# Performance work log

Measured on AMD Instinct MI355X. Metric: run time of the kernel, lower is better.

Reference implementation:

```python
import jax, jax.numpy as jnp
import numpy as np

TINY = 1e-6

def _norm(x):
    return x / (jnp.linalg.norm(x, axis=-1, keepdims=True) + TINY)

def setup_inputs() -> dict:
    key = jax.random.key(0)
    ks = jax.random.split(key, 8)
    N, L, S, H = 8192, 128, 8, 16
    points = jax.random.normal(ks[0], (N, 3), dtype=jnp.float32)
    normals = _norm(jax.random.normal(ks[1], (N, 3), dtype=jnp.float32))
    # orthonormal root rotation (world -> canonical)
    root_rot, _ = jnp.linalg.qr(jax.random.normal(ks[2], (3, 3), dtype=jnp.float32))
    lgtSGLobes = jax.random.normal(ks[3], (L, 3), dtype=jnp.float32)
    # SG sharpness must be > 1 so arccos(1 - 1/lambda) is well defined
    lgtSGLambdas = jax.random.uniform(ks[4], (L, 1), dtype=jnp.float32) * 30.0 + 5.0
    r_theta_random = jax.random.uniform(ks[5], (N, L, S), dtype=jnp.float32)
    W1 = jax.random.normal(ks[6], (6, H), dtype=jnp.float32) * 0.5
    b1 = jnp.zeros((H,), dtype=jnp.float32)
    W2 = jax.random.normal(ks[7], (H, 1), dtype=jnp.float32) * 0.5
    b2 = jnp.zeros((1,), dtype=jnp.float32)
    return {"points": points, "normals": normals, "root_rot": root_rot,
            "lgtSGLobes": lgtSGLobes, "lgtSGLambdas": lgtSGLambdas,
            "r_theta_random": r_theta_random, "W1": W1, "b1": b1, "W2": W2, "b2": b2}

def reference(points, normals, root_rot, lgtSGLobes, lgtSGLambdas,
              r_theta_random, W1, b1, W2, b2):
    # points/normals: [N,3]; lgtSGLobes: [L,3]; r_theta_random: [N,L,S]
    N = points.shape[0]
    L, S = r_theta_random.shape[1], r_theta_random.shape[2]
    l = _norm(lgtSGLobes)                                  # [L,3] SG lobe axes
    z = jnp.zeros_like(l).at[:, 2].set(1.0)
    U = _norm(jnp.cross(z, l))                             # local frame around lobe
    V = _norm(jnp.cross(l, U))
    sharp = lgtSGLambdas[:, 0]                             # [L]
    r_phi = jnp.clip(jnp.arccos(1.0 - 1.0 / sharp), None, np.pi / 3.0)  # [L]
    lin = (jnp.arange(S, dtype=points.dtype) / S)          # stratified offsets
    r_theta = (r_theta_random / S + lin) * (2.0 * np.pi)   # [N,L,S]
    st, ct = jnp.sin(r_theta), jnp.cos(r_theta)            # [N,L,S]
    sp, cp = jnp.sin(r_phi), jnp.cos(r_phi)                # [L]
    # importance-sampled directions around each lobe: [N,L,S,3]
    sample_dir = (U[None, :, None, :] * (ct * sp[None, :, None])[..., None]
                  + V[None, :, None, :] * (st * sp[None, :, None])[..., None]
                  + l[None, :, None, :] * cp[None, :, None, None])
    # hemisphere mask (normals . sample_dir > eps)
    cos_term = jnp.einsum('nd,nlsd->nls', normals, sample_dir) > TINY
    # rotate query dirs to canonical frame: (-dir) @ root_rot
    input_dir = jnp.einsum('nlsd,de->nlse', -sample_dir, root_rot)
    # visibility MLP on (point, dir); concat avoided by splitting W1
    h = jax.nn.relu(jnp.einsum('nlsd,dh->nlsh', input_dir, W1[3:])
                    + (points @ W1[:3])[:, None, None, :] + b1)   # [N,L,S,H]
    pred_vis = jax.nn.sigmoid(jnp.einsum('nlsh,ho->nlso', h, W2)[..., 0] + b2[0])
    vis = jnp.where(cos_term, pred_vis, 0.0)               # masked scatter-back
    # SG weights exp(lambda*(dir.lobe - 1)); weighted reduction over samples
    w = jnp.exp(sharp[None, :, None] * (jnp.einsum('nlsd,ld->nls', sample_dir, l) - 1.0))
    return jnp.sum(vis * w, axis=-1) / (jnp.sum(w, axis=-1) + TINY)  # [N,L]
```

## Files before the change

kernel.cpp:

```cpp
#include <hip/hip_runtime.h>
#include <math.h>

typedef _Float16 h2 __attribute__((ext_vector_type(2)));
typedef __fp16  hh2 __attribute__((ext_vector_type(2)));

constexpr int Lc = 128;
constexpr int Sc = 8;
constexpr int F0_OFF = 3072;
constexpr int F1_OFF = 3584;
constexpr int WQ_OFF = 4096;
constexpr int W2_OFF = 4224;
constexpr int B2_OFF = 4232;
constexpr int PB_OFF = 4352;

static __device__ __forceinline__ h2 pk(float a, float b) {
    return __builtin_bit_cast(h2, __builtin_amdgcn_cvt_pkrtz(a, b));
}
static __device__ __forceinline__ h2 u2h(unsigned u) {
    return __builtin_bit_cast(h2, u);
}
static __device__ __forceinline__ unsigned h2u(h2 v) {
    return __builtin_bit_cast(unsigned, v);
}
static __device__ __forceinline__ float fdot2f(h2 a, h2 b, float c) {
#if __has_builtin(__builtin_amdgcn_fdot2)
    return __builtin_amdgcn_fdot2(__builtin_bit_cast(hh2, a),
                                  __builtin_bit_cast(hh2, b), c, false);
#else
    return c + (float)a.x * (float)b.x + (float)a.y * (float)b.y;
#endif
}
static __device__ __forceinline__ float fast_exp2(float x) {
#if __has_builtin(__builtin_amdgcn_exp2f)
    return __builtin_amdgcn_exp2f(x);
#else
    return exp2f(x);
#endif
}

__global__ __launch_bounds__(256) void precompute(
    const float* __restrict__ points,
    const float* __restrict__ root_rot,
    const float* __restrict__ lobes,
    const float* __restrict__ lambdas,
    const float* __restrict__ W1,
    const float* __restrict__ b1,
    const float* __restrict__ W2,
    const float* __restrict__ b2,
    unsigned* __restrict__ ws, int N)
{
    int g = blockIdx.x * 256 + threadIdx.x;

    if (g < N) {
        float px = points[3*g], py = points[3*g+1], pz = points[3*g+2];
        unsigned* dst = ws + PB_OFF + 8*(size_t)g;
        #pragma unroll
        for (int k = 0; k < 8; ++k) {
            int h0 = 2*k, h1 = 2*k+1;
            float v0 = b1[h0] + px*W1[h0] + py*W1[16+h0] + pz*W1[32+h0];
            float v1 = b1[h1] + px*W1[h1] + py*W1[16+h1] + pz*W1[32+h1];
            dst[k] = h2u(pk(v0, v1));
        }
    }

    if (g < Lc) {
        int li = g;
        float lx = lobes[li*3+0], ly = lobes[li*3+1], lz = lobes[li*3+2];
        float inv = 1.0f / (sqrtf(lx*lx + ly*ly + lz*lz) + 1e-6f);
        lx *= inv; ly *= inv; lz *= inv;

        float ux = -ly, uy = lx;
        inv = 1.0f / (sqrtf(ux*ux + uy*uy) + 1e-6f);
        ux *= inv; uy *= inv;

        float vx = -lz*uy, vy = lz*ux, vz = lx*uy - ly*ux;
        inv = 1.0f / (sqrtf(vx*vx + vy*vy + vz*vz) + 1e-6f);
        vx *= inv; vy *= inv; vz *= inv;

        float sharp = lambdas[li];
        float cp = fmaxf(1.0f - 1.0f/sharp, 0.5f);
        float sp = sqrtf(fmaxf(1.0f - cp*cp, 0.0f));

        float uxs = ux*sp, uys = uy*sp;
        float vxs = vx*sp, vys = vy*sp, vzs = vz*sp;
        float lxc = lx*cp, lyc = ly*cp, lzc = lz*cp;

        const float r0 = root_rot[0], r1 = root_rot[1], r2 = root_rot[2];
        const float r3 = root_rot[3], r4 = root_rot[4], r5 = root_rot[5];
        const float r6 = root_rot[6], r7 = root_rot[7], r8 = root_rot[8];

        float Ur0 = -(uxs*r0 + uys*r3);
        float Ur1 = -(uxs*r1 + uys*r4);
        float Ur2 = -(uxs*r2 + uys*r5);
        float Vr0 = -(vxs*r0 + vys*r3 + vzs*r6);
        float Vr1 = -(vxs*r1 + vys*r4 + vzs*r7);
        float Vr2 = -(vxs*r2 + vys*r5 + vzs*r8);
        float Lr0 = -(lxc*r0 + lyc*r3 + lzc*r6);
        float Lr1 = -(lxc*r1 + lyc*r4 + lzc*r7);
        float Lr2 = -(lxc*r2 + lyc*r5 + lzc*r8);

        unsigned abd[24];
        #pragma unroll
        for (int k = 0; k < 8; ++k) {
            int h0 = 2*k, h1 = 2*k + 1;
            float a0 = Ur0*W1[48+h0] + Ur1*W1[64+h0] + Ur2*W1[80+h0];
            float a1 = Ur0*W1[48+h1] + Ur1*W1[64+h1] + Ur2*W1[80+h1];
            float bb0 = Vr0*W1[48+h0] + Vr1*W1[64+h0] + Vr2*W1[80+h0];
            float bb1 = Vr0*W1[48+h1] + Vr1*W1[64+h1] + Vr2*W1[80+h1];
            float d0 = Lr0*W1[48+h0] + Lr1*W1[64+h0] + Lr2*W1[80+h0];
            float d1 = Lr0*W1[48+h1] + Lr1*W1[64+h1] + Lr2*W1[80+h1];
            abd[k]      = h2u(pk(a0, a1));
            abd[8 + k]  = h2u(pk(bb0, bb1));
            abd[16 + k] = h2u(pk(d0, d1));
        }
        uint4* tv = (uint4*)ws;
        #pragma unroll
        for (int c = 0; c < 6; ++c)
            tv[c*128 + li] = *(const uint4*)(abd + 4*c);

        float* wf = (float*)ws;
        *(float4*)(wf + F0_OFF + 4*li) = (float4){uxs, uys, vxs, vys};
        *(float4*)(wf + F1_OFF + 4*li) = (float4){vzs, lxc, lyc, lzc};
        float wq = __expf(sharp * (cp - 1.0f));
        wf[WQ_OFF + li] = wq / (8.0f * wq + 1e-6f);

        if (li == 0) {
            #pragma unroll
            for (int k = 0; k < 8; ++k)
                ws[W2_OFF + k] = h2u(pk(W2[2*k], W2[2*k+1]));
            wf[B2_OFF] = -b2[0] * 1.44269504f;
        }
    }
}

__global__ __launch_bounds__(256, 4) void vis_main(
    const float* __restrict__ normals,
    const float* __restrict__ rtheta,
    const unsigned* __restrict__ ws,
    float* __restrict__ out, int N)
{
    int idx = blockIdx.x * 256 + threadIdx.x;
    if (idx >= N * Lc) return;
    int n  = idx >> 7;
    int li = idx & (Lc - 1);

    const uint4* tv = (const uint4*)ws;
    uint4 a01 = tv[0*128 + li];
    uint4 a23 = tv[1*128 + li];
    uint4 bb01 = tv[2*128 + li];
    uint4 bb23 = tv[3*128 + li];
    uint4 d01 = tv[4*128 + li];
    uint4 d23 = tv[5*128 + li];
    const float* wf = (const float*)ws;
    float4 f0 = *(const float4*)(wf + F0_OFF + 4*li);
    float4 f1 = *(const float4*)(wf + F1_OFF + 4*li);
    float wqp = wf[WQ_OFF + li];

    const float4 q0 = *reinterpret_cast<const float4*>(rtheta + (size_t)idx * Sc);
    const float4 q1 = *reinterpret_cast<const float4*>(rtheta + (size_t)idx * Sc + 4);
    float rs[Sc] = {q0.x, q0.y, q0.z, q0.w, q1.x, q1.y, q1.z, q1.w};

    int nu = __builtin_amdgcn_readfirstlane(n);
    const float* nn = normals + 3*(size_t)nu;
    float nx = nn[0], ny = nn[1], nz = nn[2];
    const unsigned* pbp = ws + PB_OFF + 8*(size_t)nu;
    unsigned pb[8] = {pbp[0], pbp[1], pbp[2], pbp[3],
                      pbp[4], pbp[5], pbp[6], pbp[7]};

    h2 A[8] = {u2h(a01.x), u2h(a01.y), u2h(a01.z), u2h(a01.w),
               u2h(a23.x), u2h(a23.y), u2h(a23.z), u2h(a23.w)};
    h2 B[8] = {u2h(bb01.x), u2h(bb01.y), u2h(bb01.z), u2h(bb01.w),
               u2h(bb23.x), u2h(bb23.y), u2h(bb23.z), u2h(bb23.w)};
    h2 G[8] = {u2h(pb[0]) + u2h(d01.x), u2h(pb[1]) + u2h(d01.y),
               u2h(pb[2]) + u2h(d01.z), u2h(pb[3]) + u2h(d01.w),
               u2h(pb[4]) + u2h(d23.x), u2h(pb[5]) + u2h(d23.y),
               u2h(pb[6]) + u2h(d23.z), u2h(pb[7]) + u2h(d23.w)};
    h2 W2h[8] = {u2h(ws[W2_OFF+0]), u2h(ws[W2_OFF+1]),
                 u2h(ws[W2_OFF+2]), u2h(ws[W2_OFF+3]),
                 u2h(ws[W2_OFF+4]), u2h(ws[W2_OFF+5]),
                 u2h(ws[W2_OFF+6]), u2h(ws[W2_OFF+7])};
    float b2c = wf[B2_OFF];

    float nU = nx*f0.x + ny*f0.y;
    float nV = nx*f0.z + ny*f0.w + nz*f1.x;
    float nL = nx*f1.y + ny*f1.z + nz*f1.w;

    const h2 zero = {(_Float16)0.0f, (_Float16)0.0f};
    float svis = 0.0f;
    #pragma unroll
    for (int s = 0; s < Sc; ++s) {
        float f  = fmaf(rs[s], 0.125f, (float)s * 0.125f);
        float st = __builtin_amdgcn_sinf(f);
        float ct = __builtin_amdgcn_cosf(f);
        float ndot = fmaf(ct, nU, fmaf(st, nV, nL));

        h2 ct2 = pk(ct, ct);
        h2 st2 = pk(st, st);

        float acc = 0.0f;
        #pragma unroll
        for (int k = 0; k < 8; ++k) {
            h2 hv = __builtin_elementwise_fma(ct2, A[k],
                     __builtin_elementwise_fma(st2, B[k], G[k]));
            hv = __builtin_elementwise_max(hv, zero);
            acc = fdot2f(hv, W2h[k], acc);
        }
        float e = fast_exp2(fmaf(acc, -1.44269504f, b2c));
        float pred = __builtin_amdgcn_rcpf(1.0f + e);
        svis += (ndot > 1e-6f) ? pred : 0.0f;
    }

    out[idx] = svis * wqp;
}

extern "C" void kernel_launch(void* const* d_in, const int* in_sizes, int n_in,
                              void* d_out, int out_size, void* d_ws, size_t ws_size,
                              hipStream_t stream) {
    const float* points  = (const float*)d_in[0];
    const float* normals = (const float*)d_in[1];
    const float* root_rot= (const float*)d_in[2];
    const float* lobes   = (const float*)d_in[3];
    const float* lambdas = (const float*)d_in[4];
    const float* rtheta  = (const float*)d_in[5];
    const float* W1      = (const float*)d_in[6];
    const float* b1      = (const float*)d_in[7];
    const float* W2      = (const float*)d_in[8];
    const float* b2      = (const float*)d_in[9];
    float* out = (float*)d_out;
    unsigned* ws = (unsigned*)d_ws;

    int N = in_sizes[0] / 3;
    int total = N * Lc;

    int pre_blocks = (N + 255) / 256;
    precompute<<<pre_blocks, 256, 0, stream>>>(points, root_rot, lobes, lambdas,
                                               W1, b1, W2, b2, ws, N);
    vis_main<<<(total + 255) / 256, 256, 0, stream>>>(normals, rtheta, ws, out, N);
}
```

Before: 24.88 us.

## Fuse precompute into main kernel with per-block LDS tables

Removes the separate precompute launch. Each block now recomputes the per-lobe frame and MLP projection tables into shared memory, splitting the hidden units across its two halves, plus the point bias for its two points. The main computation then reads these tables from LDS instead of a global workspace. This drops one kernel launch and the global round trip, at the cost of redundant per-block setup work (lobe normalization and W1 projections in every block) and a __syncthreads barrier.

```diff
diff --git a/kernel.cpp b/kernel.cpp
--- a/kernel.cpp
+++ b/kernel.cpp
@@ -6,12 +6,11 @@
 
 constexpr int Lc = 128;
 constexpr int Sc = 8;
-constexpr int F0_OFF = 3072;
-constexpr int F1_OFF = 3584;
+
+constexpr int F_OFF  = 3072;
 constexpr int WQ_OFF = 4096;
-constexpr int W2_OFF = 4224;
-constexpr int B2_OFF = 4232;
-constexpr int PB_OFF = 4352;
+constexpr int PB_OFF = 4224;
+constexpr int LDS_DW = 4240;
 
 static __device__ __forceinline__ h2 pk(float a, float b) {
     return __builtin_bit_cast(h2, __builtin_amdgcn_cvt_pkrtz(a, b));
@@ -38,33 +37,24 @@
 #endif
 }
 
-__global__ __launch_bounds__(256) void precompute(
+__global__ __launch_bounds__(256, 4) void vis_fused(
     const float* __restrict__ points,
+    const float* __restrict__ normals,
     const float* __restrict__ root_rot,
     const float* __restrict__ lobes,
     const float* __restrict__ lambdas,
+    const float* __restrict__ rtheta,
     const float* __restrict__ W1,
     const float* __restrict__ b1,
     const float* __restrict__ W2,
     const float* __restrict__ b2,
-    unsigned* __restrict__ ws, int N)
+    float* __restrict__ out, int N)
 {
-    int g = blockIdx.x * 256 + threadIdx.x;
-
-    if (g < N) {
-        float px = points[3*g], py = points[3*g+1], pz = points[3*g+2];
-        unsigned* dst = ws + PB_OFF + 8*(size_t)g;
-        #pragma unroll
-        for (int k = 0; k < 8; ++k) {
-            int h0 = 2*k, h1 = 2*k+1;
-            float v0 = b1[h0] + px*W1[h0] + py*W1[16+h0] + pz*W1[32+h0];
-            float v1 = b1[h1] + px*W1[h1] + py*W1[16+h1] + pz*W1[32+h1];
-            dst[k] = h2u(pk(v0, v1));
-        }
-    }
-
-    if (g < Lc) {
-        int li = g;
+    __shared__ __align__(16) unsigned lds[LDS_DW];
+    const int tid = threadIdx.x;
+    const int li  = tid & (Lc - 1);
+
+    {
         float lx = lobes[li*3+0], ly = lobes[li*3+1], lz = lobes[li*3+2];
         float inv = 1.0f / (sqrtf(lx*lx + ly*ly + lz*lz) + 1e-6f);
         lx *= inv; ly *= inv; lz *= inv;
@@ -99,61 +89,66 @@
         float Lr1 = -(lxc*r1 + lyc*r4 + lzc*r7);
         float Lr2 = -(lxc*r2 + lyc*r5 + lzc*r8);
 
-        unsigned abd[24];
+        const int k0 = (tid < 128) ? 0 : 4;
+        unsigned av[4], bv[4], dv[4];
         #pragma unroll
-        for (int k = 0; k < 8; ++k) {
-            int h0 = 2*k, h1 = 2*k + 1;
-            float a0 = Ur0*W1[48+h0] + Ur1*W1[64+h0] + Ur2*W1[80+h0];
-            float a1 = Ur0*W1[48+h1] + Ur1*W1[64+h1] + Ur2*W1[80+h1];
+        for (int j = 0; j < 4; ++j) {
+            int h0 = 2*(k0 + j), h1 = h0 + 1;
+            float a0  = Ur0*W1[48+h0] + Ur1*W1[64+h0] + Ur2*W1[80+h0];
+            float a1  = Ur0*W1[48+h1] + Ur1*W1[64+h1] + Ur2*W1[80+h1];
             float bb0 = Vr0*W1[48+h0] + Vr1*W1[64+h0] + Vr2*W1[80+h0];
             float bb1 = Vr0*W1[48+h1] + Vr1*W1[64+h1] + Vr2*W1[80+h1];
-            float d0 = Lr0*W1[48+h0] + Lr1*W1[64+h0] + Lr2*W1[80+h0];
-            float d1 = Lr0*W1[48+h1] + Lr1*W1[64+h1] + Lr2*W1[80+h1];
-            abd[k]      = h2u(pk(a0, a1));
-            abd[8 + k]  = h2u(pk(bb0, bb1));
-            abd[16 + k] = h2u(pk(d0, d1));
-        }
-        uint4* tv = (uint4*)ws;
+            float d0  = Lr0*W1[48+h0] + Lr1*W1[64+h0] + Lr2*W1[80+h0];
+            float d1  = Lr0*W1[48+h1] + Lr1*W1[64+h1] + Lr2*W1[80+h1];
+            av[j] = h2u(pk(a0, a1));
+            bv[j] = h2u(pk(bb0, bb1));
+            dv[j] = h2u(pk(d0, d1));
+        }
         #pragma unroll
-        for (int c = 0; c < 6; ++c)
-            tv[c*128 + li] = *(const uint4*)(abd + 4*c);
-
-        float* wf = (float*)ws;
-        *(float4*)(wf + F0_OFF + 4*li) = (float4){uxs, uys, vxs, vys};
-        *(float4*)(wf + F1_OFF + 4*li) = (float4){vzs, lxc, lyc, lzc};
-        float wq = __expf(sharp * (cp - 1.0f));
-        wf[WQ_OFF + li] = wq / (8.0f * wq + 1e-6f);
-
-        if (li == 0) {
-            #pragma unroll
-            for (int k = 0; k < 8; ++k)
-                ws[W2_OFF + k] = h2u(pk(W2[2*k], W2[2*k+1]));
-            wf[B2_OFF] = -b2[0] * 1.44269504f;
+        for (int j = 0; j < 4; j += 2) {
+            int g = (k0 + j) >> 1;
+            *(uint2*)(lds + (0*4 + g)*256 + li*2) = (uint2){av[j], av[j+1]};
+            *(uint2*)(lds + (1*4 + g)*256 + li*2) = (uint2){bv[j], bv[j+1]};
+            *(uint2*)(lds + (2*4 + g)*256 + li*2) = (uint2){dv[j], dv[j+1]};
+        }
+
+        float* wf = (float*)lds;
+        if (tid < 128) {
+            *(float2*)(wf + F_OFF + 0*256 + li*2) = (float2){uxs, uys};
+            *(float2*)(wf + F_OFF + 1*256 + li*2) = (float2){vxs, vys};
+            *(float2*)(wf + F_OFF + 2*256 + li*2) = (float2){vzs, lxc};
+            *(float2*)(wf + F_OFF + 3*256 + li*2) = (float2){lyc, lzc};
+            float wq = __expf(sharp * (cp - 1.0f));
+            wf[WQ_OFF + li] = wq / (8.0f * wq + 1e-6f);
+        } else if (tid < 130) {
+            int p = (blockIdx.x << 1) + (tid - 128);
+            if (p < N) {
+                float px = points[3*p], py = points[3*p+1], pz = points[3*p+2];
+                #pragma unroll
+                for (int k = 0; k < 8; ++k) {
+                    int h0 = 2*k, h1 = 2*k + 1;
+                    float v0 = b1[h0] + px*W1[h0] + py*W1[16+h0] + pz*W1[32+h0];
+                    float v1 = b1[h1] + px*W1[h1] + py*W1[16+h1] + pz*W1[32+h1];
+                    lds[PB_OFF + (tid - 128)*8 + k] = h2u(pk(v0, v1));
+                }
+            }
         }
     }
-}
-
-__global__ __launch_bounds__(256, 4) void vis_main(
-    const float* __restrict__ normals,
-    const float* __restrict__ rtheta,
-    const unsigned* __restrict__ ws,
-    float* __restrict__ out, int N)
-{
-    int idx = blockIdx.x * 256 + threadIdx.x;
+    __syncthreads();
+
+    const int idx = blockIdx.x * 256 + tid;
     if (idx >= N * Lc) return;
-    int n  = idx >> 7;
-    int li = idx & (Lc - 1);
-
-    const uint4* tv = (const uint4*)ws;
-    uint4 a01 = tv[0*128 + li];
-    uint4 a23 = tv[1*128 + li];
-    uint4 bb01 = tv[2*128 + li];
-    uint4 bb23 = tv[3*128 + li];
-    uint4 d01 = tv[4*128 + li];
-    uint4 d23 = tv[5*128 + li];
-    const float* wf = (const float*)ws;
-    float4 f0 = *(const float4*)(wf + F0_OFF + 4*li);
-    float4 f1 = *(const float4*)(wf + F1_OFF + 4*li);
+    const int n = (blockIdx.x << 1) + (tid >> 7);
+
+    uint2 t[12];
+    #pragma unroll
+    for (int g = 0; g < 12; ++g)
+        t[g] = *(const uint2*)(lds + g*256 + li*2);
+    const float* wf = (const float*)lds;
+    float2 g0 = *(const float2*)(wf + F_OFF + 0*256 + li*2);
+    float2 g1 = *(const float2*)(wf + F_OFF + 1*256 + li*2);
+    float2 g2 = *(const float2*)(wf + F_OFF + 2*256 + li*2);
+    float2 g3 = *(const float2*)(wf + F_OFF + 3*256 + li*2);
     float wqp = wf[WQ_OFF + li];
 
     const float4 q0 = *reinterpret_cast<const float4*>(rtheta + (size_t)idx * Sc);
@@ -163,27 +158,25 @@
     int nu = __builtin_amdgcn_readfirstlane(n);
     const float* nn = normals + 3*(size_t)nu;
     float nx = nn[0], ny = nn[1], nz = nn[2];
-    const unsigned* pbp = ws + PB_OFF + 8*(size_t)nu;
-    unsigned pb[8] = {pbp[0], pbp[1], pbp[2], pbp[3],
-                      pbp[4], pbp[5], pbp[6], pbp[7]};
-
-    h2 A[8] = {u2h(a01.x), u2h(a01.y), u2h(a01.z), u2h(a01.w),
-               u2h(a23.x), u2h(a23.y), u2h(a23.z), u2h(a23.w)};
-    h2 B[8] = {u2h(bb01.x), u2h(bb01.y), u2h(bb01.z), u2h(bb01.w),
-               u2h(bb23.x), u2h(bb23.y), u2h(bb23.z), u2h(bb23.w)};
-    h2 G[8] = {u2h(pb[0]) + u2h(d01.x), u2h(pb[1]) + u2h(d01.y),
-               u2h(pb[2]) + u2h(d01.z), u2h(pb[3]) + u2h(d01.w),
-               u2h(pb[4]) + u2h(d23.x), u2h(pb[5]) + u2h(d23.y),
-               u2h(pb[6]) + u2h(d23.z), u2h(pb[7]) + u2h(d23.w)};
-    h2 W2h[8] = {u2h(ws[W2_OFF+0]), u2h(ws[W2_OFF+1]),
-                 u2h(ws[W2_OFF+2]), u2h(ws[W2_OFF+3]),
-                 u2h(ws[W2_OFF+4]), u2h(ws[W2_OFF+5]),
-                 u2h(ws[W2_OFF+6]), u2h(ws[W2_OFF+7])};
-    float b2c = wf[B2_OFF];
-
-    float nU = nx*f0.x + ny*f0.y;
-    float nV = nx*f0.z + ny*f0.w + nz*f1.x;
-    float nL = nx*f1.y + ny*f1.z + nz*f1.w;
+    const unsigned* pbp = lds + PB_OFF + (tid >> 7)*8;
+
+    h2 A[8] = {u2h(t[0].x), u2h(t[0].y), u2h(t[1].x), u2h(t[1].y),
+               u2h(t[2].x), u2h(t[2].y), u2h(t[3].x), u2h(t[3].y)};
+    h2 B[8] = {u2h(t[4].x), u2h(t[4].y), u2h(t[5].x), u2h(t[5].y),
+               u2h(t[6].x), u2h(t[6].y), u2h(t[7].x), u2h(t[7].y)};
+    h2 G[8] = {u2h(pbp[0]) + u2h(t[8].x),  u2h(pbp[1]) + u2h(t[8].y),
+               u2h(pbp[2]) + u2h(t[9].x),  u2h(pbp[3]) + u2h(t[9].y),
+               u2h(pbp[4]) + u2h(t[10].x), u2h(pbp[5]) + u2h(t[10].y),
+               u2h(pbp[6]) + u2h(t[11].x), u2h(pbp[7]) + u2h(t[11].y)};
+
+    h2 W2h[8];
+    #pragma unroll
+    for (int k = 0; k < 8; ++k) W2h[k] = pk(W2[2*k], W2[2*k+1]);
+    float b2c = -b2[0] * 1.44269504f;
+
+    float nU = nx*g0.x + ny*g0.y;
+    float nV = nx*g1.x + ny*g1.y + nz*g2.x;
+    float nL = nx*g2.y + ny*g3.x + nz*g3.y;
 
     const h2 zero = {(_Float16)0.0f, (_Float16)0.0f};
     float svis = 0.0f;
@@ -227,13 +220,11 @@
     const float* W2      = (const float*)d_in[8];
     const float* b2      = (const float*)d_in[9];
     float* out = (float*)d_out;
-    unsigned* ws = (unsigned*)d_ws;
+    (void)d_ws; (void)ws_size;
 
     int N = in_sizes[0] / 3;
     int total = N * Lc;
-
-    int pre_blocks = (N + 255) / 256;
-    precompute<<<pre_blocks, 256, 0, stream>>>(points, root_rot, lobes, lambdas,
-                                               W1, b1, W2, b2, ws, N);
-    vis_main<<<(total + 255) / 256, 256, 0, stream>>>(normals, rtheta, ws, out, N);
-}
+    vis_fused<<<(total + 255) / 256, 256, 0, stream>>>(
+        points, normals, root_rot, lobes, lambdas, rtheta,
+        W1, b1, W2, b2, out, N);
+}
```

Result: slower. 26.52 us (+6.6%).
